# Optimization experiments

Measured on AMD Instinct MI355X. Metric: run time of the kernel, lower is better.

Reference implementation:

```python
import jax, jax.numpy as jnp
import numpy as np

B, N, M, K, C = 2, 4096, 4096, 32, 64
RADIUS = 0.08


def _ball_query(d2, radius, k):
    # d2: (B, N, M) squared distances. Returns (B, N, k) int32 indices of the
    # first k in-radius neighbors (in index order); empty slots are filled with
    # the first found neighbor (or 0 if none), matching standard ball_query.
    m = d2.shape[-1]
    mask = d2 < radius * radius
    ar = jnp.arange(m, dtype=jnp.int32)
    key = jnp.where(mask, ar, ar + m)          # in-radius indices sort first
    neg_vals, _ = jax.lax.top_k(-key, k)       # k smallest keys
    vals = -neg_vals
    valid = vals < m
    raw = vals % m
    fill = raw[..., :1]                        # first neighbor (0 if none)
    return jnp.where(valid, raw, fill)


def setup_inputs() -> dict:
    key = jax.random.key(0)
    ks = jax.random.split(key, 9)
    points = jax.random.uniform(ks[0], (B, 3, N), dtype=jnp.float32)
    knnpoints = jax.random.uniform(ks[1], (B, 3, M), dtype=jnp.float32)
    feat = jax.random.normal(ks[2], (B, C, M), dtype=jnp.float32)
    w1 = jax.random.normal(ks[3], (128, C + 4), dtype=jnp.float32) * 0.05
    b1 = jnp.zeros((128,), jnp.float32)
    w2 = jax.random.normal(ks[4], (64, 128), dtype=jnp.float32) * 0.05
    b2 = jnp.zeros((64,), jnp.float32)
    w3 = jax.random.normal(ks[5], (64, 64), dtype=jnp.float32) * 0.05
    b3 = jnp.zeros((64,), jnp.float32)
    return {"points": points, "knnpoints": knnpoints, "feat": feat,
            "w1": w1, "b1": b1, "w2": w2, "b2": b2, "w3": w3, "b3": b3}


def reference(points, knnpoints, feat, w1, b1, w2, b2, w3, b3):
    # pairwise squared distances (B, N, M), computed once and reused by
    # ball_query and ChamferLoss
    pe = jnp.sum(points ** 2, axis=1)                       # (B, N)
    ke = jnp.sum(knnpoints ** 2, axis=1)                    # (B, M)
    cross = jnp.einsum('bdn,bdm->bnm', points, knnpoints)
    d2 = jnp.maximum(pe[:, :, None] + ke[:, None, :] - 2.0 * cross, 0.0)

    idx = _ball_query(jax.lax.stop_gradient(d2), RADIUS, K)  # (B, N, K)

    # gather neighbor coords / features: knnpoints[j, :, idx[j]]
    nb = jax.vmap(lambda p, i: p[:, i])(knnpoints, idx)      # (B, 3, N, K)
    nf = jax.vmap(lambda f, i: f[:, i])(feat, idx)           # (B, C, N, K)

    # relation features (neighbor_feature): diff + squared distance
    diff = nb - points[:, :, :, None]                        # (B, 3, N, K)
    dist = jnp.sum(diff ** 2, axis=1, keepdims=True)         # (B, 1, N, K)
    x = jnp.concatenate([nf, diff, dist], axis=1)            # (B, C+4, N, K)

    # SharedMLP: 1x1 conv stacks + ReLU
    h = jax.nn.relu(jnp.einsum('oc,bcnk->bonk', w1, x) + b1[None, :, None, None])
    h = jax.nn.relu(jnp.einsum('oc,bcnk->bonk', w2, h) + b2[None, :, None, None])
    h = jax.nn.relu(jnp.einsum('oc,bcnk->bonk', w3, h) + b3[None, :, None, None])
    agg = jnp.sum(h, axis=3)                                 # (B, 64, N)

    # ChamferLoss between points and knnpoints
    cd = jnp.sqrt(1e-6 + d2)
    loss = jnp.min(cd, axis=1).mean() + jnp.min(cd, axis=2).mean()
    return agg, loss
```

## Files before the change

### kernel.cpp

```cpp
#include <hip/hip_runtime.h>
#include <cstdint>

#define BB 2
#define NN 4096
#define MM 4096
#define KK 32
#define CC 64
#define R2C 0.0064f

typedef _Float16 v8h __attribute__((ext_vector_type(8)));
typedef _Float16 v4h __attribute__((ext_vector_type(4)));
typedef float    v4f __attribute__((ext_vector_type(4)));

#define H1S 136
#define H2S 72

#define NBLK_COLMIN 512
#define NBLK_HEAVY  512
#define NBLK_TOTAL  1024

__launch_bounds__(256)
__global__ void prep_kernel(const float* __restrict__ knn,
                            const float* __restrict__ feat,
                            const float* __restrict__ w1,
                            const float* __restrict__ w2,
                            const float* __restrict__ w3,
                            _Float16* __restrict__ featH,
                            _Float16* __restrict__ w1h,
                            _Float16* __restrict__ w2h,
                            _Float16* __restrict__ w3h,
                            float4* __restrict__ knnP) {
    __shared__ float tl[64][17];
    int t = threadIdx.x, blk = blockIdx.x;

    if (blk < 512) {
        int b = blk >> 8;
        int tb = blk & 255;
        int c0 = (tb >> 6) * 16;
        int m0 = (tb & 63) * 64;
        const float* src = feat + (size_t)b * CC * MM;
        int mi = t & 63, cg = t >> 6;
#pragma unroll
        for (int r = 0; r < 4; ++r) {
            int cl = cg * 4 + r;
            tl[mi][cl] = src[(size_t)(c0 + cl) * MM + m0 + mi];
        }
        __syncthreads();
        int mm2 = t >> 2, j4 = (t & 3) * 4;
        _Float16* dst = featH + ((size_t)b * MM + m0 + mm2) * CC + c0 + j4;
        v4h v;
#pragma unroll
        for (int j = 0; j < 4; ++j) v[j] = (_Float16)tl[mm2][j4 + j];
        *(v4h*)dst = v;
    } else if (blk < 560) {
        int tt = (blk - 512) * 256 + t;
        if (tt < 128 * 96) {
            int r = tt / 96, k = tt - r * 96;
            w1h[tt] = (_Float16)((k < 68) ? w1[r * 68 + k] : 0.0f);
        }
        if (tt < 64 * 128) w2h[tt] = (_Float16)w2[tt];
        if (tt < 64 * 64)  w3h[tt] = (_Float16)w3[tt];
    } else {
        int i0 = (blk - 560) * 256 + t;
#pragma unroll
        for (int j = 0; j < 4; ++j) {
            int i = i0 + 2048 * j;
            int b = i >> 12, m = i & (MM - 1);
            const float* kp = knn + (size_t)b * 3 * MM;
            float x = kp[m], y = kp[MM + m], z = kp[2 * MM + m];
            float e = __fadd_rn(__fadd_rn(__fmul_rn(x, x), __fmul_rn(y, y)),
                                __fmul_rn(z, z));
            knnP[i] = make_float4(x, y, z, e);
        }
    }
}

__launch_bounds__(256, 4)
__global__ void fused_kernel(const float* __restrict__ points,
                             const float4* __restrict__ knnP,
                             const _Float16* __restrict__ featH,
                             const _Float16* __restrict__ w1h, const float* __restrict__ b1,
                             const _Float16* __restrict__ w2h, const float* __restrict__ b2,
                             const _Float16* __restrict__ w3h, const float* __restrict__ b3,
                             float* __restrict__ lossbuf,
                             float* __restrict__ out) {
    __shared__ __align__(16) _Float16 SM[64 * H1S + 64 * H2S];
    _Float16* H1 = SM;
    _Float16* H2 = SM + 64 * H1S;
    __shared__ int    sidx_f[16][KK];
    __shared__ v4h    meta[16][KK];
    __shared__ float4 Plds[16];
    __shared__ float  ws4[4];

    int t = threadIdx.x;
    int w = t >> 6, lane = t & 63;
    int blk = blockIdx.x;

    if (blk < NBLK_COLMIN) {
        float4* tile = (float4*)SM;
        int m0 = blk * 16;
        int b = blk >> 8;
        const float* pp = points + (size_t)b * 3 * NN;
        const float4* kq = knnP + (size_t)b * MM;
        float4 Kp[4];
#pragma unroll
        for (int p = 0; p < 4; ++p)
            Kp[p] = kq[(m0 & (MM - 1)) + 4 * w + p];
        float mn[4] = {1e30f, 1e30f, 1e30f, 1e30f};

        for (int ch = 0; ch < 4; ++ch) {
            const float* px = pp + ch * 1024;
#pragma unroll
            for (int j = 0; j < 4; ++j) {
                int i = t + 256 * j;
                float x = px[i], y = px[NN + i], z = px[2 * NN + i];
                float e = __fadd_rn(__fadd_rn(__fmul_rn(x, x), __fmul_rn(y, y)),
                                    __fmul_rn(z, z));
                tile[i] = make_float4(x, y, z, e);
            }
            __syncthreads();
#pragma unroll 2
            for (int i = 0; i < 16; ++i) {
                float4 p4 = tile[i * 64 + lane];
#pragma unroll
                for (int p = 0; p < 4; ++p) {
                    float cross = __builtin_fmaf(p4.z, Kp[p].z,
                                  __builtin_fmaf(p4.y, Kp[p].y,
                                                 __fmul_rn(p4.x, Kp[p].x)));
                    float d2 = __fsub_rn(__fadd_rn(p4.w, Kp[p].w),
                                         __fmul_rn(2.0f, cross));
                    mn[p] = fminf(mn[p], d2);
                }
            }
            __syncthreads();
        }

        float lsum = 0.0f;
#pragma unroll
        for (int p = 0; p < 4; ++p) {
            float mv = mn[p];
            for (int off = 32; off > 0; off >>= 1)
                mv = fminf(mv, __shfl_xor(mv, off));
            lsum += sqrtf(1e-6f + fmaxf(mv, 0.0f));
        }
        if (lane == 0) ws4[w] = lsum;
        __syncthreads();
        if (t == 0)
            lossbuf[blk] = (ws4[0] + ws4[1] + ws4[2] + ws4[3])
                           * (1.0f / (BB * MM));
    } else {
        int pt0 = (blk - NBLK_COLMIN) * 16;
        int b = pt0 >> 12;
        int n0 = pt0 & (NN - 1);
        const float* pp = points + (size_t)b * 3 * NN;
        const float4* kq = knnP + (size_t)b * MM;

        int quad = lane >> 4, lc = lane & 15;

        v8h a1[2][3], a2[4], a3[2];
#pragma unroll
        for (int rt = 0; rt < 2; ++rt)
#pragma unroll
            for (int ks = 0; ks < 3; ++ks)
                a1[rt][ks] = *(const v8h*)(w1h + (32 * w + 16 * rt + lc) * 96 + 32 * ks + 8 * quad);
#pragma unroll
        for (int ks = 0; ks < 4; ++ks)
            a2[ks] = *(const v8h*)(w2h + (16 * w + lc) * 128 + 32 * ks + 8 * quad);
#pragma unroll
        for (int ks = 0; ks < 2; ++ks)
            a3[ks] = *(const v8h*)(w3h + (16 * w + lc) * 64 + 32 * ks + 8 * quad);

        v4f bias1a = *(const v4f*)(b1 + 32 * w + 4 * quad);
        v4f bias1b = *(const v4f*)(b1 + 32 * w + 16 + 4 * quad);
        v4f bias2  = *(const v4f*)(b2 + 16 * w + 4 * quad);
        v4f bias3  = *(const v4f*)(b3 + 16 * w + 4 * quad);

        float4 P[4];
#pragma unroll
        for (int p = 0; p < 4; ++p) {
            int nl = n0 + 4 * w + p;
            float x = pp[nl], y = pp[NN + nl], z = pp[2 * NN + nl];
            float e = __fadd_rn(__fadd_rn(__fmul_rn(x, x), __fmul_rn(y, y)),
                                __fmul_rn(z, z));
            P[p] = make_float4(x, y, z, e);
        }
        if (lane == 0) {
#pragma unroll
            for (int p = 0; p < 4; ++p) Plds[4 * w + p] = P[p];
        }

        float4* tile = (float4*)SM;
        int cnt[4] = {0, 0, 0, 0};
        float mn[4] = {1e30f, 1e30f, 1e30f, 1e30f};

        for (int ch = 0; ch < 4; ++ch) {
#pragma unroll
            for (int j = 0; j < 4; ++j) {
                int i = t + 256 * j;
                tile[i] = kq[ch * 1024 + i];
            }
            __syncthreads();
#pragma unroll 2
            for (int i = 0; i < 16; ++i) {
                float4 k4 = tile[i * 64 + lane];
                int m = ch * 1024 + i * 64 + lane;
#pragma unroll
                for (int p = 0; p < 4; ++p) {
                    float cross = __builtin_fmaf(P[p].z, k4.z,
                                  __builtin_fmaf(P[p].y, k4.y,
                                                 __fmul_rn(P[p].x, k4.x)));
                    float d2 = __fsub_rn(__fadd_rn(P[p].w, k4.w),
                                         __fmul_rn(2.0f, cross));
                    mn[p] = fminf(mn[p], d2);
                    bool hit = d2 < R2C;
                    unsigned long long mask = __ballot(hit);
                    if (mask) {
                        if (hit) {
                            int pos = cnt[p] + __builtin_amdgcn_mbcnt_hi(
                                         (unsigned)(mask >> 32),
                                         __builtin_amdgcn_mbcnt_lo((unsigned)mask, 0));
                            if (pos < KK) sidx_f[4 * w + p][pos] = m;
                        }
                        cnt[p] += __popcll(mask);
                    }
                }
            }
            __syncthreads();
        }

        float lsum = 0.0f;
#pragma unroll
        for (int p = 0; p < 4; ++p) {
            int row = 4 * w + p;
            if (lane < KK) {
                int fillv = (cnt[p] > 0) ? sidx_f[row][0] : 0;
                int v = (lane < cnt[p]) ? sidx_f[row][lane] : fillv;
                sidx_f[row][lane] = v;
            }
            float mv = mn[p];
            for (int off = 32; off > 0; off >>= 1)
                mv = fminf(mv, __shfl_xor(mv, off));
            lsum += sqrtf(1e-6f + fmaxf(mv, 0.0f));
        }
        if (lane == 0) ws4[w] = lsum;
        __syncthreads();
        if (t == 0)
            lossbuf[blk] = (ws4[0] + ws4[1] + ws4[2] + ws4[3])
                           * (1.0f / (BB * NN));

#pragma unroll
        for (int c = t; c < 512; c += 256) {
            int row = c >> 5, kk = c & 31;
            int id = sidx_f[row][kk];
            float4 k4 = kq[id];
            float4 Pm = Plds[row];
            float dx = k4.x - Pm.x, dy = k4.y - Pm.y, dz = k4.z - Pm.z;
            float dd = __fadd_rn(__fadd_rn(__fmul_rn(dx, dx), __fmul_rn(dy, dy)),
                                 __fmul_rn(dz, dz));
            v4h mv;
            mv[0] = (_Float16)dx; mv[1] = (_Float16)dy;
            mv[2] = (_Float16)dz; mv[3] = (_Float16)dd;
            meta[row][kk] = mv;
        }
        __syncthreads();

        for (int q = 0; q < 8; ++q) {
#pragma unroll 2
            for (int ct = 0; ct < 4; ++ct) {
                int colb = 16 * ct + lc;
                int row = 2 * q + (ct >> 1);
                int kk = colb & 31;
                int id = sidx_f[row][kk];
                const _Float16* frow = featH + ((size_t)(b * MM + id)) * CC;
                v8h bx0 = *(const v8h*)(frow + 8 * quad);
                v8h bx1 = *(const v8h*)(frow + 32 + 8 * quad);
                v4h mr = meta[row][kk];
                v8h bx2 = {(_Float16)0.f, (_Float16)0.f, (_Float16)0.f, (_Float16)0.f,
                           (_Float16)0.f, (_Float16)0.f, (_Float16)0.f, (_Float16)0.f};
                if (quad == 0) {
                    bx2[0] = mr[0]; bx2[1] = mr[1];
                    bx2[2] = mr[2]; bx2[3] = mr[3];
                }
                v4f acc0 = bias1a, acc1 = bias1b;
                acc0 = __builtin_amdgcn_mfma_f32_16x16x32_f16(a1[0][0], bx0, acc0, 0, 0, 0);
                acc1 = __builtin_amdgcn_mfma_f32_16x16x32_f16(a1[1][0], bx0, acc1, 0, 0, 0);
                acc0 = __builtin_amdgcn_mfma_f32_16x16x32_f16(a1[0][1], bx1, acc0, 0, 0, 0);
                acc1 = __builtin_amdgcn_mfma_f32_16x16x32_f16(a1[1][1], bx1, acc1, 0, 0, 0);
                acc0 = __builtin_amdgcn_mfma_f32_16x16x32_f16(a1[0][2], bx2, acc0, 0, 0, 0);
                acc1 = __builtin_amdgcn_mfma_f32_16x16x32_f16(a1[1][2], bx2, acc1, 0, 0, 0);
                v4h h0, h1v;
#pragma unroll
                for (int r = 0; r < 4; ++r) {
                    h0[r]  = (_Float16)fmaxf(acc0[r], 0.0f);
                    h1v[r] = (_Float16)fmaxf(acc1[r], 0.0f);
                }
                *(v4h*)(H1 + colb * H1S + 32 * w + 4 * quad)      = h0;
                *(v4h*)(H1 + colb * H1S + 32 * w + 16 + 4 * quad) = h1v;
            }
            __syncthreads();

#pragma unroll 1
            for (int ct = 0; ct < 4; ++ct) {
                int colb = 16 * ct + lc;
                v4f acc = bias2;
#pragma unroll
                for (int ks = 0; ks < 4; ++ks) {
                    v8h bx = *(const v8h*)(H1 + colb * H1S + 32 * ks + 8 * quad);
                    acc = __builtin_amdgcn_mfma_f32_16x16x32_f16(a2[ks], bx, acc, 0, 0, 0);
                }
                v4h h;
#pragma unroll
                for (int r = 0; r < 4; ++r) h[r] = (_Float16)fmaxf(acc[r], 0.0f);
                *(v4h*)(H2 + colb * H2S + 16 * w + 4 * quad) = h;
            }
            __syncthreads();

#pragma unroll 1
            for (int p = 0; p < 2; ++p) {
                int cA = (2 * p) * 16 + lc, cB = (2 * p + 1) * 16 + lc;
                v4f accA = bias3, accB = bias3;
#pragma unroll
                for (int ks = 0; ks < 2; ++ks) {
                    v8h bA = *(const v8h*)(H2 + cA * H2S + 32 * ks + 8 * quad);
                    v8h bB = *(const v8h*)(H2 + cB * H2S + 32 * ks + 8 * quad);
                    accA = __builtin_amdgcn_mfma_f32_16x16x32_f16(a3[ks], bA, accA, 0, 0, 0);
                    accB = __builtin_amdgcn_mfma_f32_16x16x32_f16(a3[ks], bB, accB, 0, 0, 0);
                }
                v4f s;
#pragma unroll
                for (int r = 0; r < 4; ++r)
                    s[r] = fmaxf(accA[r], 0.0f) + fmaxf(accB[r], 0.0f);
#pragma unroll
                for (int off = 1; off < 16; off <<= 1) {
#pragma unroll
                    for (int r = 0; r < 4; ++r) s[r] += __shfl_xor(s[r], off);
                }
                if (lc == 0) {
                    int n = n0 + 2 * q + p;
                    int rowb = 16 * w + 4 * quad;
#pragma unroll
                    for (int r = 0; r < 4; ++r)
                        out[((size_t)(b * 64 + rowb + r)) * NN + n] = s[r];
                }
            }
            __syncthreads();
        }
    }
}

__launch_bounds__(256)
__global__ void loss_kernel(const float* __restrict__ lossbuf,
                            float* __restrict__ out) {
    __shared__ float ws4[4];
    int t = threadIdx.x;
    float s = 0.0f;
#pragma unroll
    for (int q = 0; q < 4; ++q)
        s += lossbuf[t + 256 * q];
    for (int off = 32; off > 0; off >>= 1) s += __shfl_xor(s, off);
    if ((t & 63) == 0) ws4[t >> 6] = s;
    __syncthreads();
    if (t == 0)
        out[(size_t)BB * 64 * NN] = ws4[0] + ws4[1] + ws4[2] + ws4[3];
}

extern "C" void kernel_launch(void* const* d_in, const int* in_sizes, int n_in,
                              void* d_out, int out_size, void* d_ws, size_t ws_size,
                              hipStream_t stream) {
    const float* points = (const float*)d_in[0];
    const float* knn    = (const float*)d_in[1];
    const float* feat   = (const float*)d_in[2];
    const float* w1 = (const float*)d_in[3];
    const float* b1 = (const float*)d_in[4];
    const float* w2 = (const float*)d_in[5];
    const float* b2 = (const float*)d_in[6];
    const float* w3 = (const float*)d_in[7];
    const float* b3 = (const float*)d_in[8];
    float* out = (float*)d_out;

    char* ws = (char*)d_ws;
    _Float16*  featH   = (_Float16*)ws;
    _Float16*  w1h     = (_Float16*)(ws + 1048576);
    _Float16*  w2h     = (_Float16*)(ws + 1073152);
    _Float16*  w3h     = (_Float16*)(ws + 1089536);
    float4*    knnP    = (float4*)(ws + 1097728);
    float*     lossbuf = (float*)(ws + 1228800);

    prep_kernel<<<568, 256, 0, stream>>>(knn, feat, w1, w2, w3,
                                         featH, w1h, w2h, w3h, knnP);
    fused_kernel<<<NBLK_TOTAL, 256, 0, stream>>>(points, knnP, featH,
                                                 w1h, b1, w2h, b2, w3h, b3,
                                                 lossbuf, out);
    loss_kernel<<<1, 256, 0, stream>>>(lossbuf, out);
}
```

Before: 122.5 us.

## Halve points per heavy block, drop LDS tiling, prefetch neighbor features

Heavy blocks now handle 8 query points instead of 16, which doubles their count and reorders the blocks so heavy ones come first, followed by the column-min blocks. The ball-query scan reads knnP directly from global memory instead of staging tiles in LDS, removing the per-chunk syncthreads. The MLP loop software-prefetches the gathered neighbor features for the next group while the current one is computed, and drops the trailing barrier. Occupancy is raised to 5 blocks per SM. The risks are redundant global reads of knnP, since each block now scans all of M for fewer points, and possible hazards from the removed barrier.

```diff
diff --git a/kernel.cpp b/kernel.cpp
--- a/kernel.cpp
+++ b/kernel.cpp
@@ -15,9 +15,9 @@
 #define H1S 136
 #define H2S 72
 
+#define NBLK_HEAVY  1024
 #define NBLK_COLMIN 512
-#define NBLK_HEAVY  512
-#define NBLK_TOTAL  1024
+#define NBLK_TOTAL  1536
 
 __launch_bounds__(256)
 __global__ void prep_kernel(const float* __restrict__ knn,
@@ -75,7 +75,7 @@
     }
 }
 
-__launch_bounds__(256, 4)
+__launch_bounds__(256, 5)
 __global__ void fused_kernel(const float* __restrict__ points,
                              const float4* __restrict__ knnP,
                              const _Float16* __restrict__ featH,
@@ -87,19 +87,20 @@
     __shared__ __align__(16) _Float16 SM[64 * H1S + 64 * H2S];
     _Float16* H1 = SM;
     _Float16* H2 = SM + 64 * H1S;
-    __shared__ int    sidx_f[16][KK];
-    __shared__ v4h    meta[16][KK];
-    __shared__ float4 Plds[16];
+    __shared__ int    sidx_f[8][KK];
+    __shared__ v4h    meta[8][KK];
+    __shared__ float4 Plds[8];
     __shared__ float  ws4[4];
 
     int t = threadIdx.x;
     int w = t >> 6, lane = t & 63;
     int blk = blockIdx.x;
 
-    if (blk < NBLK_COLMIN) {
+    if (blk >= NBLK_HEAVY) {
+        int cb = blk - NBLK_HEAVY;
         float4* tile = (float4*)SM;
-        int m0 = blk * 16;
-        int b = blk >> 8;
+        int m0 = cb * 16;
+        int b = cb >> 8;
         const float* pp = points + (size_t)b * 3 * NN;
         const float4* kq = knnP + (size_t)b * MM;
         float4 Kp[4];
@@ -149,7 +150,7 @@
             lossbuf[blk] = (ws4[0] + ws4[1] + ws4[2] + ws4[3])
                            * (1.0f / (BB * MM));
     } else {
-        int pt0 = (blk - NBLK_COLMIN) * 16;
+        int pt0 = blk * 8;
         int b = pt0 >> 12;
         int n0 = pt0 & (NN - 1);
         const float* pp = points + (size_t)b * 3 * NN;
@@ -175,63 +176,49 @@
         v4f bias2  = *(const v4f*)(b2 + 16 * w + 4 * quad);
         v4f bias3  = *(const v4f*)(b3 + 16 * w + 4 * quad);
 
-        float4 P[4];
-#pragma unroll
-        for (int p = 0; p < 4; ++p) {
-            int nl = n0 + 4 * w + p;
+        float4 P[2];
+#pragma unroll
+        for (int p = 0; p < 2; ++p) {
+            int nl = n0 + 2 * w + p;
             float x = pp[nl], y = pp[NN + nl], z = pp[2 * NN + nl];
             float e = __fadd_rn(__fadd_rn(__fmul_rn(x, x), __fmul_rn(y, y)),
                                 __fmul_rn(z, z));
             P[p] = make_float4(x, y, z, e);
         }
-        if (lane == 0) {
-#pragma unroll
-            for (int p = 0; p < 4; ++p) Plds[4 * w + p] = P[p];
-        }
-
-        float4* tile = (float4*)SM;
-        int cnt[4] = {0, 0, 0, 0};
-        float mn[4] = {1e30f, 1e30f, 1e30f, 1e30f};
-
-        for (int ch = 0; ch < 4; ++ch) {
-#pragma unroll
-            for (int j = 0; j < 4; ++j) {
-                int i = t + 256 * j;
-                tile[i] = kq[ch * 1024 + i];
-            }
-            __syncthreads();
-#pragma unroll 2
-            for (int i = 0; i < 16; ++i) {
-                float4 k4 = tile[i * 64 + lane];
-                int m = ch * 1024 + i * 64 + lane;
-#pragma unroll
-                for (int p = 0; p < 4; ++p) {
-                    float cross = __builtin_fmaf(P[p].z, k4.z,
-                                  __builtin_fmaf(P[p].y, k4.y,
-                                                 __fmul_rn(P[p].x, k4.x)));
-                    float d2 = __fsub_rn(__fadd_rn(P[p].w, k4.w),
-                                         __fmul_rn(2.0f, cross));
-                    mn[p] = fminf(mn[p], d2);
-                    bool hit = d2 < R2C;
-                    unsigned long long mask = __ballot(hit);
-                    if (mask) {
-                        if (hit) {
-                            int pos = cnt[p] + __builtin_amdgcn_mbcnt_hi(
-                                         (unsigned)(mask >> 32),
-                                         __builtin_amdgcn_mbcnt_lo((unsigned)mask, 0));
-                            if (pos < KK) sidx_f[4 * w + p][pos] = m;
-                        }
-                        cnt[p] += __popcll(mask);
+        if (lane == 0) { Plds[2 * w] = P[0]; Plds[2 * w + 1] = P[1]; }
+
+        int cnt[2] = {0, 0};
+        float mn[2] = {1e30f, 1e30f};
+#pragma unroll 4
+        for (int it = 0; it < 64; ++it) {
+            int m = it * 64 + lane;
+            float4 k4 = kq[m];
+#pragma unroll
+            for (int p = 0; p < 2; ++p) {
+                float cross = __builtin_fmaf(P[p].z, k4.z,
+                              __builtin_fmaf(P[p].y, k4.y,
+                                             __fmul_rn(P[p].x, k4.x)));
+                float d2 = __fsub_rn(__fadd_rn(P[p].w, k4.w),
+                                     __fmul_rn(2.0f, cross));
+                mn[p] = fminf(mn[p], d2);
+                bool hit = d2 < R2C;
+                unsigned long long mask = __ballot(hit);
+                if (mask) {
+                    if (hit) {
+                        int pos = cnt[p] + __builtin_amdgcn_mbcnt_hi(
+                                     (unsigned)(mask >> 32),
+                                     __builtin_amdgcn_mbcnt_lo((unsigned)mask, 0));
+                        if (pos < KK) sidx_f[2 * w + p][pos] = m;
                     }
-                }
-            }
-            __syncthreads();
+                    cnt[p] += __popcll(mask);
+                }
+            }
         }
 
         float lsum = 0.0f;
 #pragma unroll
-        for (int p = 0; p < 4; ++p) {
-            int row = 4 * w + p;
+        for (int p = 0; p < 2; ++p) {
+            int row = 2 * w + p;
             if (lane < KK) {
                 int fillv = (cnt[p] > 0) ? sidx_f[row][0] : 0;
                 int v = (lane < cnt[p]) ? sidx_f[row][lane] : fillv;
@@ -248,9 +235,8 @@
             lossbuf[blk] = (ws4[0] + ws4[1] + ws4[2] + ws4[3])
                            * (1.0f / (BB * NN));
 
-#pragma unroll
-        for (int c = t; c < 512; c += 256) {
-            int row = c >> 5, kk = c & 31;
+        {
+            int row = t >> 5, kk = t & 31;
             int id = sidx_f[row][kk];
             float4 k4 = kq[id];
             float4 Pm = Plds[row];
@@ -264,17 +250,28 @@
         }
         __syncthreads();
 
-        for (int q = 0; q < 8; ++q) {
-#pragma unroll 2
+        v8h pf0[4], pf1[4];
+        v4h pfm[4];
+        auto prefetch = [&](int q) {
+#pragma unroll
             for (int ct = 0; ct < 4; ++ct) {
                 int colb = 16 * ct + lc;
-                int row = 2 * q + (ct >> 1);
-                int kk = colb & 31;
+                int row = 2 * q + (ct >> 1), kk = colb & 31;
                 int id = sidx_f[row][kk];
                 const _Float16* frow = featH + ((size_t)(b * MM + id)) * CC;
-                v8h bx0 = *(const v8h*)(frow + 8 * quad);
-                v8h bx1 = *(const v8h*)(frow + 32 + 8 * quad);
-                v4h mr = meta[row][kk];
+                pf0[ct] = *(const v8h*)(frow + 8 * quad);
+                pf1[ct] = *(const v8h*)(frow + 32 + 8 * quad);
+                pfm[ct] = meta[row][kk];
+            }
+        };
+        prefetch(0);
+
+        for (int q = 0; q < 4; ++q) {
+#pragma unroll
+            for (int ct = 0; ct < 4; ++ct) {
+                int colb = 16 * ct + lc;
+                v8h bx0 = pf0[ct], bx1 = pf1[ct];
+                v4h mr = pfm[ct];
                 v8h bx2 = {(_Float16)0.f, (_Float16)0.f, (_Float16)0.f, (_Float16)0.f,
                            (_Float16)0.f, (_Float16)0.f, (_Float16)0.f, (_Float16)0.f};
                 if (quad == 0) {
@@ -297,6 +294,7 @@
                 *(v4h*)(H1 + colb * H1S + 32 * w + 4 * quad)      = h0;
                 *(v4h*)(H1 + colb * H1S + 32 * w + 16 + 4 * quad) = h1v;
             }
+            if (q < 3) prefetch(q + 1);
             __syncthreads();
 
 #pragma unroll 1
@@ -343,7 +341,6 @@
                         out[((size_t)(b * 64 + rowb + r)) * NN + n] = s[r];
                 }
             }
-            __syncthreads();
         }
     }
 }
@@ -355,7 +352,7 @@
     int t = threadIdx.x;
     float s = 0.0f;
 #pragma unroll
-    for (int q = 0; q < 4; ++q)
+    for (int q = 0; q < 6; ++q)
         s += lossbuf[t + 256 * q];
     for (int off = 32; off > 0; off >>= 1) s += __shfl_xor(s, off);
     if ((t & 63) == 0) ws4[t >> 6] = s;
```

After: 193.3 us. +57.8%, slower.
